# Kernel tuning notes

Hardware: AMD Instinct MI355X
Metric: run time of the kernel (lower is better)

## Reference

```python
import jax, jax.numpy as jnp
import numpy as np

N, M, D = 100000, 50000, 256


def setup_inputs() -> dict:
    key = jax.random.key(0)
    k1, k2, k3 = jax.random.split(key, 3)
    self_tensor = jax.random.normal(k1, (N, D), dtype=jnp.float32)
    updates = jax.random.normal(k2, (M, D), dtype=jnp.float32)
    index = jax.random.randint(k3, (M, D), 0, N, dtype=jnp.int32)
    return {"self_tensor": self_tensor, "index": index, "updates": updates, "axis": 0}


def reference(self_tensor, index, updates, axis):
    # torch.scatter_add(out, 0, index, updates):
    #   out[index[i, j], j] += updates[i, j]
    assert axis == 0, "reference implements scatter along axis 0"
    m, d = index.shape
    cols = jnp.broadcast_to(jnp.arange(d, dtype=index.dtype)[None, :], (m, d))
    return self_tensor.at[index, cols].add(updates)
```

## Files before the change

kernel.cpp:

```cpp
#include <hip/hip_runtime.h>

#define DCOLS 256
#define RB 128
#define NBIN_PAD 1024
#define PAIRS_OFF 16384
#define CHUNK4 4096
#define SUB4 1024
#define NSUB (CHUNK4 / SUB4)

typedef unsigned int u32;
typedef unsigned short u16;
typedef unsigned long long u64;

__global__ void copy_f4(const float4* __restrict__ src, float4* __restrict__ dst, int n4) {
    int i = blockIdx.x * blockDim.x + threadIdx.x;
    int stride = gridDim.x * blockDim.x;
    for (; i < n4; i += stride) dst[i] = src[i];
}

__global__ void scatter_add4(const int4* __restrict__ index,
                             const float4* __restrict__ upd,
                             float* __restrict__ out, int n4) {
    int i = blockIdx.x * blockDim.x + threadIdx.x;
    int stride = gridDim.x * blockDim.x;
    for (; i < n4; i += stride) {
        int4 idx  = index[i];
        float4 u  = upd[i];
        int j = (i << 2) & (DCOLS - 1);
        atomicAdd(&out[idx.x * DCOLS + j + 0], u.x);
        atomicAdd(&out[idx.y * DCOLS + j + 1], u.y);
        atomicAdd(&out[idx.z * DCOLS + j + 2], u.z);
        atomicAdd(&out[idx.w * DCOLS + j + 3], u.w);
    }
}

__global__ void zero_meta(u32* __restrict__ count, int nbins) {
    int i = threadIdx.x;
    if (i < nbins) count[i] = 0;
}

__global__ void __launch_bounds__(256) count_bins(const int4* __restrict__ idx4,
                                                  u32* __restrict__ count, int n4) {
    __shared__ u32 hist[NBIN_PAD];
    for (int i = threadIdx.x; i < NBIN_PAD; i += blockDim.x) hist[i] = 0;
    __syncthreads();
    int i = blockIdx.x * blockDim.x + threadIdx.x;
    int stride = gridDim.x * blockDim.x;
    for (; i < n4; i += stride) {
        int4 v = idx4[i];
        atomicAdd(&hist[((u32)v.x) >> 7], 1u);
        atomicAdd(&hist[((u32)v.y) >> 7], 1u);
        atomicAdd(&hist[((u32)v.z) >> 7], 1u);
        atomicAdd(&hist[((u32)v.w) >> 7], 1u);
    }
    __syncthreads();
    for (int i2 = threadIdx.x; i2 < NBIN_PAD; i2 += blockDim.x)
        if (hist[i2]) atomicAdd(&count[i2], hist[i2]);
}

__global__ void scan_bins(const u32* __restrict__ count, u32* __restrict__ start,
                          u32* __restrict__ cursor, int nbins) {
    __shared__ u32 tmp[1024];
    int t = threadIdx.x;
    u32 v = (t < nbins) ? count[t] : 0u;
    tmp[t] = v;
    __syncthreads();
    for (int off = 1; off < 1024; off <<= 1) {
        u32 a = 0;
        if (t >= off) a = tmp[t - off];
        __syncthreads();
        tmp[t] += a;
        __syncthreads();
    }
    if (t < nbins) {
        u32 excl = tmp[t] - v;
        start[t] = excl;
        cursor[t] = excl;
    }
}

__global__ void __launch_bounds__(256) bin_scatter_v3(const int4* __restrict__ idx4,
                                                      const float4* __restrict__ upd4,
                                                      u32* __restrict__ cursor,
                                                      u64* __restrict__ pairs, int n4) {
    __shared__ u32 hist[NBIN_PAD];
    __shared__ u32 basep[NBIN_PAD];
    __shared__ u16 excl[NBIN_PAD];
    __shared__ u32 wtot[4];
    __shared__ u64 stage[SUB4 * 4];

    int t = threadIdx.x;
    int lane = t & 63, wid = t >> 6;
    int b0 = blockIdx.x * CHUNK4;

    for (int i = t; i < NBIN_PAD; i += 256) hist[i] = 0;
    __syncthreads();

#pragma unroll
    for (int k = 0; k < CHUNK4 / 256; ++k) {
        int p = b0 + t + 256 * k;
        if (p < n4) {
            int4 v = idx4[p];
            atomicAdd(&hist[((u32)v.x) >> 7], 1u);
            atomicAdd(&hist[((u32)v.y) >> 7], 1u);
            atomicAdd(&hist[((u32)v.z) >> 7], 1u);
            atomicAdd(&hist[((u32)v.w) >> 7], 1u);
        }
    }
    __syncthreads();
    for (int b = t; b < NBIN_PAD; b += 256) {
        u32 c = hist[b];
        basep[b] = c ? atomicAdd(&cursor[b], c) : 0u;
    }
    __syncthreads();

    for (int s = 0; s < NSUB; ++s) {
        int sbase = b0 + s * SUB4;
        int4 iv[4]; float4 uv[4];
#pragma unroll
        for (int k = 0; k < 4; ++k) {
            int p = sbase + t + 256 * k;
            if (p < n4) { iv[k] = idx4[p]; uv[k] = upd4[p]; }
        }
        for (int i = t; i < NBIN_PAD; i += 256) hist[i] = 0;
        __syncthreads();
#pragma unroll
        for (int k = 0; k < 4; ++k) {
            int p = sbase + t + 256 * k;
            if (p < n4) {
                atomicAdd(&hist[((u32)iv[k].x) >> 7], 1u);
                atomicAdd(&hist[((u32)iv[k].y) >> 7], 1u);
                atomicAdd(&hist[((u32)iv[k].z) >> 7], 1u);
                atomicAdd(&hist[((u32)iv[k].w) >> 7], 1u);
            }
        }
        __syncthreads();
        u32 c0 = hist[4 * t + 0], c1 = hist[4 * t + 1];
        u32 c2 = hist[4 * t + 2], c3 = hist[4 * t + 3];
        u32 tsum = c0 + c1 + c2 + c3;
        u32 incl = tsum;
#pragma unroll
        for (int d = 1; d < 64; d <<= 1) {
            u32 y = __shfl_up(incl, (unsigned)d, 64);
            if (lane >= d) incl += y;
        }
        if (lane == 63) wtot[wid] = incl;
        __syncthreads();
        u32 woff = 0;
#pragma unroll
        for (int w = 0; w < 4; ++w) woff += (w < wid) ? wtot[w] : 0u;
        u32 base = woff + incl - tsum;
        u32 e0 = base, e1 = base + c0, e2 = e1 + c1, e3 = e2 + c2;
        excl[4 * t + 0] = (u16)e0; excl[4 * t + 1] = (u16)e1;
        excl[4 * t + 2] = (u16)e2; excl[4 * t + 3] = (u16)e3;
        hist[4 * t + 0] = e0; hist[4 * t + 1] = e1;
        hist[4 * t + 2] = e2; hist[4 * t + 3] = e3;
        __syncthreads();
#pragma unroll
        for (int k = 0; k < 4; ++k) {
            int p = sbase + t + 256 * k;
            if (p >= n4) continue;
            int rows[4] = {iv[k].x, iv[k].y, iv[k].z, iv[k].w};
            float vals[4] = {uv[k].x, uv[k].y, uv[k].z, uv[k].w};
            u32 colbase = ((u32)p * 4u) & 255u;
#pragma unroll
            for (int c = 0; c < 4; ++c) {
                u32 row = (u32)rows[c];
                u32 slot = atomicAdd(&hist[row >> 7], 1u);
                stage[slot] = ((u64)__float_as_uint(vals[c]) << 32)
                            | ((u64)row << 8) | (u64)(colbase + (u32)c);
            }
        }
        __syncthreads();
        int sv = n4 - sbase; if (sv > SUB4) sv = SUB4; if (sv < 0) sv = 0;
        int scount = 4 * sv;
        for (int i = t; i < scount; i += 256) {
            u64 pr = stage[i];
            u32 rc  = (u32)pr & 0x1ffffffu;
            u32 row = rc >> 8;
            u32 bin = row >> 7;
            u32 dest = basep[bin] + ((u32)i - (u32)excl[bin]);
            u32 key = ((row & 127u) << 8) | (rc & 255u);
            pairs[dest] = (pr & 0xffffffff00000000ull) | (u64)key;
        }
        __syncthreads();
        for (int b = t; b < NBIN_PAD; b += 256) basep[b] += hist[b] - (u32)excl[b];
        __syncthreads();
    }
}

#define APPLY_P(p) { u32 k_ = (u32)(p); \
    if (((k_ >> 7) & 1u) == half) \
        atomicAdd(&acc[((k_ >> 8) & 127u) * 128u + (k_ & 127u)], \
                  __uint_as_float((u32)((p) >> 32))); }

__global__ void __launch_bounds__(1024, 8) apply_half(const float4* __restrict__ self4,
                                                      const u64* __restrict__ pairs,
                                                      const u32* __restrict__ start,
                                                      const u32* __restrict__ endc,
                                                      float4* __restrict__ out4, int nrows) {
    __shared__ float acc[RB * 128];
    int t = threadIdx.x;
    int bin = blockIdx.x >> 1;
    u32 half = blockIdx.x & 1u;
    float4* acc4 = (float4*)acc;
    for (int i = t; i < RB * 32; i += 1024) acc4[i] = make_float4(0.f, 0.f, 0.f, 0.f);
    __syncthreads();

    u32 s = start[bin], e = endc[bin];
    u32 i = s + (u32)t;
    for (; i + 3072u < e; i += 4096u) {
        u64 p0 = pairs[i];
        u64 p1 = pairs[i + 1024u];
        u64 p2 = pairs[i + 2048u];
        u64 p3 = pairs[i + 3072u];
        APPLY_P(p0); APPLY_P(p1); APPLY_P(p2); APPLY_P(p3);
    }
    for (; i < e; i += 1024u) { u64 p0 = pairs[i]; APPLY_P(p0); }
    __syncthreads();

    int r0 = bin * RB;
    int nr = nrows - r0; if (nr > RB) nr = RB;
    int tot4 = nr * 32;
    for (int i2 = t; i2 < tot4; i2 += 1024) {
        int r = i2 >> 5, c4 = i2 & 31;
        long g = (long)(r0 + r) * 64 + (long)(half * 32u) + c4;
        float4 a = self4[g];
        float4 c = acc4[(r << 5) + c4];
        a.x += c.x; a.y += c.y; a.z += c.z; a.w += c.w;
        out4[g] = a;
    }
}

extern "C" void kernel_launch(void* const* d_in, const int* in_sizes, int n_in,
                              void* d_out, int out_size, void* d_ws, size_t ws_size,
                              hipStream_t stream) {
    const float* self_t = (const float*)d_in[0];
    const int*   index  = (const int*)d_in[1];
    const float* upd    = (const float*)d_in[2];
    float* out = (float*)d_out;

    const int nd = out_size;
    const int md = in_sizes[1];
    const int nrows = nd / DCOLS;
    const int nbins = (nrows + RB - 1) / RB;

    size_t need = (size_t)PAIRS_OFF + (size_t)md * 8;
    if (ws_size < need || nbins > NBIN_PAD || (md & 3) || (nd & 3)) {
        copy_f4<<<2048, 256, 0, stream>>>((const float4*)self_t, (float4*)out, nd / 4);
        scatter_add4<<<4096, 256, 0, stream>>>((const int4*)index, (const float4*)upd, out, md / 4);
        return;
    }

    u32* count  = (u32*)d_ws;
    u32* start  = count + 1024;
    u32* cursor = count + 2048;
    u64* pairs  = (u64*)((char*)d_ws + PAIRS_OFF);
    int n4 = md / 4;

    zero_meta<<<1, 1024, 0, stream>>>(count, nbins);
    count_bins<<<1024, 256, 0, stream>>>((const int4*)index, count, n4);
    scan_bins<<<1, 1024, 0, stream>>>(count, start, cursor, nbins);
    int sblocks = (n4 + CHUNK4 - 1) / CHUNK4;
    bin_scatter_v3<<<sblocks, 256, 0, stream>>>((const int4*)index, (const float4*)upd,
                                                cursor, pairs, n4);
    apply_half<<<2 * nbins, 1024, 0, stream>>>((const float4*)self_t, pairs, start, cursor,
                                               (float4*)out, nrows);
}
```

Measured before the change: 229.8 us.

## Replace count/scan pass with fixed-capacity bins plus overflow fixup

Drops the global histogram and scan kernels by giving each 128-row bin a fixed capacity region in the workspace, with cursors initialised to bin*C. Any block whose reservation would exceed a bin's capacity writes its pairs to an overflow buffer instead, and a small fixup kernel atomically adds those pairs into the output afterwards. The scatter kernel now handles one 1024-int4 sub-chunk per block with a single local histogram and scan. This removes a full read of the index array and two launches, at the cost of a larger workspace and a possible slow path if bins overflow.

```diff
diff --git a/kernel.cpp b/kernel.cpp
--- a/kernel.cpp
+++ b/kernel.cpp
@@ -4,12 +4,11 @@
 #define RB 128
 #define NBIN_PAD 1024
 #define PAIRS_OFF 16384
-#define CHUNK4 4096
 #define SUB4 1024
-#define NSUB (CHUNK4 / SUB4)
+#define CAPC 17152u
+#define OVF_CAP (1u<<20)
 
 typedef unsigned int u32;
-typedef unsigned short u16;
 typedef unsigned long long u64;
 
 __global__ void copy_f4(const float4* __restrict__ src, float4* __restrict__ dst, int n4) {
@@ -34,6 +33,13 @@
     }
 }
 
+__global__ void zero_cap(u32* __restrict__ meta, u32 C) {
+    int t = threadIdx.x;
+    meta[1024 + t] = (u32)t * C;
+    meta[2048 + t] = (u32)t * C;
+    if (t == 0) meta[3072] = 0;
+}
+
 __global__ void zero_meta(u32* __restrict__ count, int nbins) {
     int i = threadIdx.x;
     if (i < nbins) count[i] = 0;
@@ -79,113 +85,110 @@
     }
 }
 
-__global__ void __launch_bounds__(256) bin_scatter_v3(const int4* __restrict__ idx4,
-                                                      const float4* __restrict__ upd4,
-                                                      u32* __restrict__ cursor,
-                                                      u64* __restrict__ pairs, int n4) {
+__global__ void __launch_bounds__(256, 4) scatter_v4(const int4* __restrict__ idx4,
+                                                     const float4* __restrict__ upd4,
+                                                     u32* __restrict__ cursor,
+                                                     u64* __restrict__ pairs,
+                                                     u64* __restrict__ ovf,
+                                                     u32* __restrict__ ovf_cnt,
+                                                     int n4, u32 C) {
     __shared__ u32 hist[NBIN_PAD];
-    __shared__ u32 basep[NBIN_PAD];
-    __shared__ u16 excl[NBIN_PAD];
-    __shared__ u32 wtot[4];
+    __shared__ u32 bme[NBIN_PAD];
     __shared__ u64 stage[SUB4 * 4];
 
     int t = threadIdx.x;
     int lane = t & 63, wid = t >> 6;
-    int b0 = blockIdx.x * CHUNK4;
-
+    int b0 = blockIdx.x * SUB4;
+
+    int4 iv[4]; float4 uv[4];
+#pragma unroll
+    for (int k = 0; k < 4; ++k) {
+        int p = b0 + t + 256 * k;
+        if (p < n4) { iv[k] = idx4[p]; uv[k] = upd4[p]; }
+    }
     for (int i = t; i < NBIN_PAD; i += 256) hist[i] = 0;
     __syncthreads();
 
 #pragma unroll
-    for (int k = 0; k < CHUNK4 / 256; ++k) {
+    for (int k = 0; k < 4; ++k) {
         int p = b0 + t + 256 * k;
         if (p < n4) {
-            int4 v = idx4[p];
-            atomicAdd(&hist[((u32)v.x) >> 7], 1u);
-            atomicAdd(&hist[((u32)v.y) >> 7], 1u);
-            atomicAdd(&hist[((u32)v.z) >> 7], 1u);
-            atomicAdd(&hist[((u32)v.w) >> 7], 1u);
-        }
-    }
-    __syncthreads();
-    for (int b = t; b < NBIN_PAD; b += 256) {
-        u32 c = hist[b];
-        basep[b] = c ? atomicAdd(&cursor[b], c) : 0u;
-    }
-    __syncthreads();
-
-    for (int s = 0; s < NSUB; ++s) {
-        int sbase = b0 + s * SUB4;
-        int4 iv[4]; float4 uv[4];
-#pragma unroll
-        for (int k = 0; k < 4; ++k) {
-            int p = sbase + t + 256 * k;
-            if (p < n4) { iv[k] = idx4[p]; uv[k] = upd4[p]; }
-        }
-        for (int i = t; i < NBIN_PAD; i += 256) hist[i] = 0;
-        __syncthreads();
-#pragma unroll
-        for (int k = 0; k < 4; ++k) {
-            int p = sbase + t + 256 * k;
-            if (p < n4) {
-                atomicAdd(&hist[((u32)iv[k].x) >> 7], 1u);
-                atomicAdd(&hist[((u32)iv[k].y) >> 7], 1u);
-                atomicAdd(&hist[((u32)iv[k].z) >> 7], 1u);
-                atomicAdd(&hist[((u32)iv[k].w) >> 7], 1u);
+            atomicAdd(&hist[((u32)iv[k].x) >> 7], 1u);
+            atomicAdd(&hist[((u32)iv[k].y) >> 7], 1u);
+            atomicAdd(&hist[((u32)iv[k].z) >> 7], 1u);
+            atomicAdd(&hist[((u32)iv[k].w) >> 7], 1u);
+        }
+    }
+    __syncthreads();
+
+    u32 c0 = hist[4 * t + 0], c1 = hist[4 * t + 1];
+    u32 c2 = hist[4 * t + 2], c3 = hist[4 * t + 3];
+    u32 tsum = c0 + c1 + c2 + c3;
+    u32 incl = tsum;
+#pragma unroll
+    for (int d = 1; d < 64; d <<= 1) {
+        u32 y = __shfl_up(incl, (unsigned)d, 64);
+        if (lane >= d) incl += y;
+    }
+    if (lane == 63) bme[1020 + wid] = incl;
+    __syncthreads();
+    u32 woff = 0;
+#pragma unroll
+    for (int w = 0; w < 4; ++w) woff += (w < wid) ? bme[1020 + w] : 0u;
+    u32 ebase = woff + incl - tsum;
+    u32 e[4] = {ebase, ebase + c0, ebase + c0 + c1, ebase + c0 + c1 + c2};
+    u32 cc[4] = {c0, c1, c2, c3};
+#pragma unroll
+    for (int j = 0; j < 4; ++j) {
+        u32 bin = 4 * (u32)t + j;
+        u32 c = cc[j];
+        if (c) {
+            u32 gb = atomicAdd(&cursor[bin], c);
+            u32 lim = C ? (bin + 1u) * C : 0xFFFFFFFFu;
+            u32 bm;
+            if (gb + c > lim) {
+                u32 ob = atomicAdd(ovf_cnt, c);
+                bm = (ob - e[j] + 8192u) | 0x80000000u;
+            } else {
+                bm = gb - e[j] + 8192u;
             }
-        }
-        __syncthreads();
-        u32 c0 = hist[4 * t + 0], c1 = hist[4 * t + 1];
-        u32 c2 = hist[4 * t + 2], c3 = hist[4 * t + 3];
-        u32 tsum = c0 + c1 + c2 + c3;
-        u32 incl = tsum;
-#pragma unroll
-        for (int d = 1; d < 64; d <<= 1) {
-            u32 y = __shfl_up(incl, (unsigned)d, 64);
-            if (lane >= d) incl += y;
-        }
-        if (lane == 63) wtot[wid] = incl;
-        __syncthreads();
-        u32 woff = 0;
-#pragma unroll
-        for (int w = 0; w < 4; ++w) woff += (w < wid) ? wtot[w] : 0u;
-        u32 base = woff + incl - tsum;
-        u32 e0 = base, e1 = base + c0, e2 = e1 + c1, e3 = e2 + c2;
-        excl[4 * t + 0] = (u16)e0; excl[4 * t + 1] = (u16)e1;
-        excl[4 * t + 2] = (u16)e2; excl[4 * t + 3] = (u16)e3;
-        hist[4 * t + 0] = e0; hist[4 * t + 1] = e1;
-        hist[4 * t + 2] = e2; hist[4 * t + 3] = e3;
-        __syncthreads();
-#pragma unroll
-        for (int k = 0; k < 4; ++k) {
-            int p = sbase + t + 256 * k;
-            if (p >= n4) continue;
-            int rows[4] = {iv[k].x, iv[k].y, iv[k].z, iv[k].w};
-            float vals[4] = {uv[k].x, uv[k].y, uv[k].z, uv[k].w};
-            u32 colbase = ((u32)p * 4u) & 255u;
-#pragma unroll
-            for (int c = 0; c < 4; ++c) {
-                u32 row = (u32)rows[c];
-                u32 slot = atomicAdd(&hist[row >> 7], 1u);
-                stage[slot] = ((u64)__float_as_uint(vals[c]) << 32)
-                            | ((u64)row << 8) | (u64)(colbase + (u32)c);
-            }
-        }
-        __syncthreads();
-        int sv = n4 - sbase; if (sv > SUB4) sv = SUB4; if (sv < 0) sv = 0;
-        int scount = 4 * sv;
-        for (int i = t; i < scount; i += 256) {
-            u64 pr = stage[i];
-            u32 rc  = (u32)pr & 0x1ffffffu;
-            u32 row = rc >> 8;
-            u32 bin = row >> 7;
-            u32 dest = basep[bin] + ((u32)i - (u32)excl[bin]);
+            bme[bin] = bm;
+            hist[bin] = e[j];
+        }
+    }
+    __syncthreads();
+
+    u32 colbase = ((u32)t * 4u) & 255u;
+#pragma unroll
+    for (int k = 0; k < 4; ++k) {
+        int p = b0 + t + 256 * k;
+        if (p >= n4) continue;
+        int rows[4] = {iv[k].x, iv[k].y, iv[k].z, iv[k].w};
+        float vals[4] = {uv[k].x, uv[k].y, uv[k].z, uv[k].w};
+#pragma unroll
+        for (int c = 0; c < 4; ++c) {
+            u32 row = (u32)rows[c];
+            u32 slot = atomicAdd(&hist[row >> 7], 1u);
+            stage[slot] = ((u64)__float_as_uint(vals[c]) << 32)
+                        | ((u64)row << 8) | (u64)(colbase + (u32)c);
+        }
+    }
+    __syncthreads();
+
+    int scount = 4 * (n4 - b0); if (scount > 4 * SUB4) scount = 4 * SUB4;
+    for (int i = t; i < scount; i += 256) {
+        u64 pr = stage[i];
+        u32 rc  = (u32)pr & 0x1ffffffu;
+        u32 row = rc >> 8;
+        u32 bin = row >> 7;
+        u32 v = bme[bin];
+        u32 d = (v & 0x7fffffffu) + (u32)i - 8192u;
+        if (v & 0x80000000u) {
+            if (d < OVF_CAP) ovf[d] = pr;
+        } else {
             u32 key = ((row & 127u) << 8) | (rc & 255u);
-            pairs[dest] = (pr & 0xffffffff00000000ull) | (u64)key;
-        }
-        __syncthreads();
-        for (int b = t; b < NBIN_PAD; b += 256) basep[b] += hist[b] - (u32)excl[b];
-        __syncthreads();
+            pairs[d] = (pr & 0xffffffff00000000ull) | (u64)key;
+        }
     }
 }
 
@@ -198,7 +201,8 @@
                                                       const u64* __restrict__ pairs,
                                                       const u32* __restrict__ start,
                                                       const u32* __restrict__ endc,
-                                                      float4* __restrict__ out4, int nrows) {
+                                                      float4* __restrict__ out4,
+                                                      int nrows, u32 C) {
     __shared__ float acc[RB * 128];
     int t = threadIdx.x;
     int bin = blockIdx.x >> 1;
@@ -208,6 +212,7 @@
     __syncthreads();
 
     u32 s = start[bin], e = endc[bin];
+    if (C) { u32 lim = ((u32)bin + 1u) * C; if (e > lim) e = lim; }
     u32 i = s + (u32)t;
     for (; i + 3072u < e; i += 4096u) {
         u64 p0 = pairs[i];
@@ -232,6 +237,18 @@
     }
 }
 
+__global__ void ovf_fixup(const u64* __restrict__ ovf, const u32* __restrict__ ovf_cnt,
+                          float* __restrict__ out) {
+    u32 n = *ovf_cnt; if (n > OVF_CAP) n = OVF_CAP;
+    u32 i = blockIdx.x * blockDim.x + threadIdx.x;
+    u32 stride = gridDim.x * blockDim.x;
+    for (; i < n; i += stride) {
+        u64 pr = ovf[i];
+        u32 rc = (u32)pr & 0x1ffffffu;
+        atomicAdd(&out[(rc >> 8) * 256u + (rc & 255u)], __uint_as_float((u32)(pr >> 32)));
+    }
+}
+
 extern "C" void kernel_launch(void* const* d_in, const int* in_sizes, int n_in,
                               void* d_out, int out_size, void* d_ws, size_t ws_size,
                               hipStream_t stream) {
@@ -244,26 +261,38 @@
     const int md = in_sizes[1];
     const int nrows = nd / DCOLS;
     const int nbins = (nrows + RB - 1) / RB;
-
-    size_t need = (size_t)PAIRS_OFF + (size_t)md * 8;
-    if (ws_size < need || nbins > NBIN_PAD || (md & 3) || (nd & 3)) {
+    int n4 = md / 4;
+
+    u32* meta   = (u32*)d_ws;
+    u32* count  = meta;
+    u32* start  = meta + 1024;
+    u32* cursor = meta + 2048;
+    u32* ovf_cnt = meta + 3072;
+    u64* pairs  = (u64*)((char*)d_ws + PAIRS_OFF);
+
+    size_t need_cap   = (size_t)PAIRS_OFF + (size_t)nbins * CAPC * 8 + (size_t)OVF_CAP * 8;
+    size_t need_exact = (size_t)PAIRS_OFF + (size_t)md * 8;
+    bool shape_ok = (nbins <= NBIN_PAD) && !(md & 3) && !(nd & 3);
+    int sblocks = (n4 + SUB4 - 1) / SUB4;
+
+    if (shape_ok && ws_size >= need_cap) {
+        u64* ovf = pairs + (size_t)nbins * CAPC;
+        zero_cap<<<1, 1024, 0, stream>>>(meta, CAPC);
+        scatter_v4<<<sblocks, 256, 0, stream>>>((const int4*)index, (const float4*)upd,
+                                                cursor, pairs, ovf, ovf_cnt, n4, CAPC);
+        apply_half<<<2 * nbins, 1024, 0, stream>>>((const float4*)self_t, pairs, start,
+                                                   cursor, (float4*)out, nrows, CAPC);
+        ovf_fixup<<<64, 256, 0, stream>>>(ovf, ovf_cnt, out);
+    } else if (shape_ok && ws_size >= need_exact) {
+        zero_meta<<<1, 1024, 0, stream>>>(count, nbins);
+        count_bins<<<1024, 256, 0, stream>>>((const int4*)index, count, n4);
+        scan_bins<<<1, 1024, 0, stream>>>(count, start, cursor, nbins);
+        scatter_v4<<<sblocks, 256, 0, stream>>>((const int4*)index, (const float4*)upd,
+                                                cursor, pairs, pairs, ovf_cnt, n4, 0u);
+        apply_half<<<2 * nbins, 1024, 0, stream>>>((const float4*)self_t, pairs, start,
+                                                   cursor, (float4*)out, nrows, 0u);
+    } else {
         copy_f4<<<2048, 256, 0, stream>>>((const float4*)self_t, (float4*)out, nd / 4);
         scatter_add4<<<4096, 256, 0, stream>>>((const int4*)index, (const float4*)upd, out, md / 4);
-        return;
-    }
-
-    u32* count  = (u32*)d_ws;
-    u32* start  = count + 1024;
-    u32* cursor = count + 2048;
-    u64* pairs  = (u64*)((char*)d_ws + PAIRS_OFF);
-    int n4 = md / 4;
-
-    zero_meta<<<1, 1024, 0, stream>>>(count, nbins);
-    count_bins<<<1024, 256, 0, stream>>>((const int4*)index, count, n4);
-    scan_bins<<<1, 1024, 0, stream>>>(count, start, cursor, nbins);
-    int sblocks = (n4 + CHUNK4 - 1) / CHUNK4;
-    bin_scatter_v3<<<sblocks, 256, 0, stream>>>((const int4*)index, (const float4*)upd,
-                                                cursor, pairs, n4);
-    apply_half<<<2 * nbins, 1024, 0, stream>>>((const float4*)self_t, pairs, start, cursor,
-                                               (float4*)out, nrows);
-}
+    }
+}
```

Measured after the change: 354.8 us. +54.4%, slower.

## Replace atomic bin cursors with per-block histogram matrix and deterministic scan

Applied to the files above, without the earlier changes.

Replaces the global count, scan and atomic-cursor reservation with a per-block, per-bin histogram matrix. A column-wise scan over that matrix plus a bin-base scan gives every block a fixed output offset per bin, so the scatter kernel no longer does global atomics and the pair order becomes deterministic. It also drops the zeroing kernel and the second full histogram pass inside the scatter kernel. In exchange it adds an extra launch and a strided column scan over a 1024xnblk matrix, which reads memory with poor locality.

```diff
diff --git a/kernel.cpp b/kernel.cpp
--- a/kernel.cpp
+++ b/kernel.cpp
@@ -2,11 +2,13 @@
 
 #define DCOLS 256
 #define RB 128
-#define NBIN_PAD 1024
-#define PAIRS_OFF 16384
-#define CHUNK4 4096
-#define SUB4 1024
-#define NSUB (CHUNK4 / SUB4)
+#define NBINP 1024
+#define MAT_OFF 16384
+#define MAT_CAP (4u<<20)
+#define PAIRS_OFF (MAT_OFF + MAT_CAP)
+#define BLK4 1024
+#define SUBS 4
+#define CHUNK4 (BLK4 * SUBS)
 
 typedef unsigned int u32;
 typedef unsigned short u16;
@@ -34,70 +36,15 @@
     }
 }
 
-__global__ void zero_meta(u32* __restrict__ count, int nbins) {
-    int i = threadIdx.x;
-    if (i < nbins) count[i] = 0;
-}
-
-__global__ void __launch_bounds__(256) count_bins(const int4* __restrict__ idx4,
-                                                  u32* __restrict__ count, int n4) {
-    __shared__ u32 hist[NBIN_PAD];
-    for (int i = threadIdx.x; i < NBIN_PAD; i += blockDim.x) hist[i] = 0;
-    __syncthreads();
-    int i = blockIdx.x * blockDim.x + threadIdx.x;
-    int stride = gridDim.x * blockDim.x;
-    for (; i < n4; i += stride) {
-        int4 v = idx4[i];
-        atomicAdd(&hist[((u32)v.x) >> 7], 1u);
-        atomicAdd(&hist[((u32)v.y) >> 7], 1u);
-        atomicAdd(&hist[((u32)v.z) >> 7], 1u);
-        atomicAdd(&hist[((u32)v.w) >> 7], 1u);
-    }
-    __syncthreads();
-    for (int i2 = threadIdx.x; i2 < NBIN_PAD; i2 += blockDim.x)
-        if (hist[i2]) atomicAdd(&count[i2], hist[i2]);
-}
-
-__global__ void scan_bins(const u32* __restrict__ count, u32* __restrict__ start,
-                          u32* __restrict__ cursor, int nbins) {
-    __shared__ u32 tmp[1024];
-    int t = threadIdx.x;
-    u32 v = (t < nbins) ? count[t] : 0u;
-    tmp[t] = v;
-    __syncthreads();
-    for (int off = 1; off < 1024; off <<= 1) {
-        u32 a = 0;
-        if (t >= off) a = tmp[t - off];
-        __syncthreads();
-        tmp[t] += a;
-        __syncthreads();
-    }
-    if (t < nbins) {
-        u32 excl = tmp[t] - v;
-        start[t] = excl;
-        cursor[t] = excl;
-    }
-}
-
-__global__ void __launch_bounds__(256) bin_scatter_v3(const int4* __restrict__ idx4,
-                                                      const float4* __restrict__ upd4,
-                                                      u32* __restrict__ cursor,
-                                                      u64* __restrict__ pairs, int n4) {
-    __shared__ u32 hist[NBIN_PAD];
-    __shared__ u32 basep[NBIN_PAD];
-    __shared__ u16 excl[NBIN_PAD];
-    __shared__ u32 wtot[4];
-    __shared__ u64 stage[SUB4 * 4];
-
-    int t = threadIdx.x;
-    int lane = t & 63, wid = t >> 6;
+__global__ void __launch_bounds__(256) hist_blocks(const int4* __restrict__ idx4,
+                                                   u32* __restrict__ mat, int n4) {
+    __shared__ u32 hist[NBINP];
+    int t = threadIdx.x;
     int b0 = blockIdx.x * CHUNK4;
-
-    for (int i = t; i < NBIN_PAD; i += 256) hist[i] = 0;
-    __syncthreads();
-
-#pragma unroll
-    for (int k = 0; k < CHUNK4 / 256; ++k) {
+    for (int i = t; i < NBINP; i += 256) hist[i] = 0;
+    __syncthreads();
+#pragma unroll
+    for (int k = 0; k < 16; ++k) {
         int p = b0 + t + 256 * k;
         if (p < n4) {
             int4 v = idx4[p];
@@ -108,21 +55,73 @@
         }
     }
     __syncthreads();
-    for (int b = t; b < NBIN_PAD; b += 256) {
-        u32 c = hist[b];
-        basep[b] = c ? atomicAdd(&cursor[b], c) : 0u;
-    }
-    __syncthreads();
-
-    for (int s = 0; s < NSUB; ++s) {
-        int sbase = b0 + s * SUB4;
+    u32 base = (u32)blockIdx.x * NBINP;
+    for (int i = t; i < NBINP; i += 256) mat[base + i] = hist[i];
+}
+
+__global__ void __launch_bounds__(64) scan_blocks(u32* __restrict__ mat,
+                                                  u32* __restrict__ total, int nblk) {
+    int bin = blockIdx.x;
+    int lane = threadIdx.x;
+    u32 carry = 0;
+    int rounds = (nblk + 63) / 64;
+    for (int r = 0; r < rounds; ++r) {
+        int blk = r * 64 + lane;
+        u32 v = (blk < nblk) ? mat[(u32)blk * NBINP + bin] : 0u;
+        u32 incl = v;
+#pragma unroll
+        for (int d = 1; d < 64; d <<= 1) {
+            u32 y = __shfl_up(incl, (unsigned)d, 64);
+            if (lane >= d) incl += y;
+        }
+        if (blk < nblk) mat[(u32)blk * NBINP + bin] = carry + incl - v;
+        carry += (u32)__shfl(incl, 63, 64);
+    }
+    if (lane == 0) total[bin] = carry;
+}
+
+__global__ void scan_binbases(const u32* __restrict__ total, u32* __restrict__ start) {
+    __shared__ u32 tmp[1024];
+    int t = threadIdx.x;
+    u32 v = total[t];
+    tmp[t] = v;
+    __syncthreads();
+    for (int off = 1; off < 1024; off <<= 1) {
+        u32 a = (t >= off) ? tmp[t - off] : 0u;
+        __syncthreads();
+        tmp[t] += a;
+        __syncthreads();
+    }
+    start[t] = tmp[t] - v;
+}
+
+__global__ void __launch_bounds__(256, 3) scatter_det(const int4* __restrict__ idx4,
+                                                      const float4* __restrict__ upd4,
+                                                      const u32* __restrict__ mat,
+                                                      const u32* __restrict__ start,
+                                                      u64* __restrict__ pairs, int n4) {
+    __shared__ u32 hist[NBINP];
+    __shared__ u32 basep[NBINP];
+    __shared__ u16 excl16[NBINP];
+    __shared__ u32 wtot[4];
+    __shared__ u64 stage[4096];
+
+    int t = threadIdx.x;
+    int lane = t & 63, wid = t >> 6;
+    int b0 = blockIdx.x * CHUNK4;
+    u32 mbase = (u32)blockIdx.x * NBINP;
+
+    for (int i = t; i < NBINP; i += 256) basep[i] = start[i] + mat[mbase + i];
+
+    for (int s = 0; s < SUBS; ++s) {
+        int sbase = b0 + s * BLK4;
         int4 iv[4]; float4 uv[4];
 #pragma unroll
         for (int k = 0; k < 4; ++k) {
             int p = sbase + t + 256 * k;
             if (p < n4) { iv[k] = idx4[p]; uv[k] = upd4[p]; }
         }
-        for (int i = t; i < NBIN_PAD; i += 256) hist[i] = 0;
+        for (int i = t; i < NBINP; i += 256) hist[i] = 0;
         __syncthreads();
 #pragma unroll
         for (int k = 0; k < 4; ++k) {
@@ -149,20 +148,20 @@
         u32 woff = 0;
 #pragma unroll
         for (int w = 0; w < 4; ++w) woff += (w < wid) ? wtot[w] : 0u;
-        u32 base = woff + incl - tsum;
-        u32 e0 = base, e1 = base + c0, e2 = e1 + c1, e3 = e2 + c2;
-        excl[4 * t + 0] = (u16)e0; excl[4 * t + 1] = (u16)e1;
-        excl[4 * t + 2] = (u16)e2; excl[4 * t + 3] = (u16)e3;
+        u32 e0 = woff + incl - tsum;
+        u32 e1 = e0 + c0, e2 = e1 + c1, e3 = e2 + c2;
+        excl16[4 * t + 0] = (u16)e0; excl16[4 * t + 1] = (u16)e1;
+        excl16[4 * t + 2] = (u16)e2; excl16[4 * t + 3] = (u16)e3;
         hist[4 * t + 0] = e0; hist[4 * t + 1] = e1;
         hist[4 * t + 2] = e2; hist[4 * t + 3] = e3;
         __syncthreads();
+        u32 colbase = (4u * (u32)t) & 255u;
 #pragma unroll
         for (int k = 0; k < 4; ++k) {
             int p = sbase + t + 256 * k;
             if (p >= n4) continue;
             int rows[4] = {iv[k].x, iv[k].y, iv[k].z, iv[k].w};
             float vals[4] = {uv[k].x, uv[k].y, uv[k].z, uv[k].w};
-            u32 colbase = ((u32)p * 4u) & 255u;
 #pragma unroll
             for (int c = 0; c < 4; ++c) {
                 u32 row = (u32)rows[c];
@@ -172,19 +171,19 @@
             }
         }
         __syncthreads();
-        int sv = n4 - sbase; if (sv > SUB4) sv = SUB4; if (sv < 0) sv = 0;
+        int sv = n4 - sbase; if (sv > BLK4) sv = BLK4; if (sv < 0) sv = 0;
         int scount = 4 * sv;
         for (int i = t; i < scount; i += 256) {
             u64 pr = stage[i];
             u32 rc  = (u32)pr & 0x1ffffffu;
             u32 row = rc >> 8;
             u32 bin = row >> 7;
-            u32 dest = basep[bin] + ((u32)i - (u32)excl[bin]);
+            u32 d = basep[bin] + ((u32)i - (u32)excl16[bin]);
             u32 key = ((row & 127u) << 8) | (rc & 255u);
-            pairs[dest] = (pr & 0xffffffff00000000ull) | (u64)key;
-        }
-        __syncthreads();
-        for (int b = t; b < NBIN_PAD; b += 256) basep[b] += hist[b] - (u32)excl[b];
+            pairs[d] = (pr & 0xffffffff00000000ull) | (u64)key;
+        }
+        __syncthreads();
+        for (int b = t; b < NBINP; b += 256) basep[b] += hist[b] - (u32)excl16[b];
         __syncthreads();
     }
 }
@@ -197,7 +196,7 @@
 __global__ void __launch_bounds__(1024, 8) apply_half(const float4* __restrict__ self4,
                                                       const u64* __restrict__ pairs,
                                                       const u32* __restrict__ start,
-                                                      const u32* __restrict__ endc,
+                                                      const u32* __restrict__ total,
                                                       float4* __restrict__ out4, int nrows) {
     __shared__ float acc[RB * 128];
     int t = threadIdx.x;
@@ -207,7 +206,7 @@
     for (int i = t; i < RB * 32; i += 1024) acc4[i] = make_float4(0.f, 0.f, 0.f, 0.f);
     __syncthreads();
 
-    u32 s = start[bin], e = endc[bin];
+    u32 s = start[bin], e = s + total[bin];
     u32 i = s + (u32)t;
     for (; i + 3072u < e; i += 4096u) {
         u64 p0 = pairs[i];
@@ -244,26 +243,28 @@
     const int md = in_sizes[1];
     const int nrows = nd / DCOLS;
     const int nbins = (nrows + RB - 1) / RB;
+    int n4 = md / 4;
+    int nblk = (n4 + CHUNK4 - 1) / CHUNK4;
+
+    u32* total = (u32*)d_ws;
+    u32* start = total + 1024;
+    u32* mat   = (u32*)((char*)d_ws + MAT_OFF);
+    u64* pairs = (u64*)((char*)d_ws + PAIRS_OFF);
 
     size_t need = (size_t)PAIRS_OFF + (size_t)md * 8;
-    if (ws_size < need || nbins > NBIN_PAD || (md & 3) || (nd & 3)) {
+    bool shape_ok = (nbins <= NBINP) && (nblk <= 1024) && !(md & 3) && !(nd & 3) &&
+                    (md % DCOLS == 0) && (nd % DCOLS == 0);
+
+    if (shape_ok && ws_size >= need) {
+        hist_blocks<<<nblk, 256, 0, stream>>>((const int4*)index, mat, n4);
+        scan_blocks<<<NBINP, 64, 0, stream>>>(mat, total, nblk);
+        scan_binbases<<<1, 1024, 0, stream>>>(total, start);
+        scatter_det<<<nblk, 256, 0, stream>>>((const int4*)index, (const float4*)upd,
+                                              mat, start, pairs, n4);
+        apply_half<<<2 * nbins, 1024, 0, stream>>>((const float4*)self_t, pairs, start,
+                                                   total, (float4*)out, nrows);
+    } else {
         copy_f4<<<2048, 256, 0, stream>>>((const float4*)self_t, (float4*)out, nd / 4);
         scatter_add4<<<4096, 256, 0, stream>>>((const int4*)index, (const float4*)upd, out, md / 4);
-        return;
-    }
-
-    u32* count  = (u32*)d_ws;
-    u32* start  = count + 1024;
-    u32* cursor = count + 2048;
-    u64* pairs  = (u64*)((char*)d_ws + PAIRS_OFF);
-    int n4 = md / 4;
-
-    zero_meta<<<1, 1024, 0, stream>>>(count, nbins);
-    count_bins<<<1024, 256, 0, stream>>>((const int4*)index, count, n4);
-    scan_bins<<<1, 1024, 0, stream>>>(count, start, cursor, nbins);
-    int sblocks = (n4 + CHUNK4 - 1) / CHUNK4;
-    bin_scatter_v3<<<sblocks, 256, 0, stream>>>((const int4*)index, (const float4*)upd,
-                                                cursor, pairs, n4);
-    apply_half<<<2 * nbins, 1024, 0, stream>>>((const float4*)self_t, pairs, start, cursor,
-                                               (float4*)out, nrows);
-}
+    }
+}
```

New measurement: 204.1 us. -11.1%, faster.
